# Optimization experiments

Measured on AMD Instinct MI355X. Metric: run time of the kernel, lower is better.

The kernel has to match this reference:

```python
import jax, jax.numpy as jnp
import numpy as np

N_HEAD = 16
D_MODEL = 1024
D_HEAD = D_MODEL // N_HEAD
B, T = 2, 2048


def setup_inputs() -> dict:
    key = jax.random.key(0)
    k1, k2, k3 = jax.random.split(key, 3)
    x = jax.random.normal(k1, (B, T, D_MODEL), dtype=jnp.float32)
    w_attn = jax.random.normal(k2, (3 * D_MODEL, D_MODEL), dtype=jnp.float32) * (D_MODEL ** -0.5)
    w_proj = jax.random.normal(k3, (D_MODEL, D_MODEL), dtype=jnp.float32) * (D_MODEL ** -0.5)
    return {"x": x, "w_attn": w_attn, "w_proj": w_proj}


def _rms_norm(x):
    eps = jnp.asarray(jnp.finfo(x.dtype).eps, x.dtype)
    var = jnp.mean(jnp.square(x), axis=-1, keepdims=True)
    return x * jax.lax.rsqrt(var + eps)


def _rotate_half(x):
    x1, x2 = jnp.split(x, 2, axis=-1)
    return jnp.concatenate((-x2, x1), axis=-1)


def reference(x, w_attn, w_proj):
    Bx, Tx, C = x.shape
    qkv = jnp.einsum('btc,fc->btf', x, w_attn)  # [B,T,3C]
    q, k, v = jnp.split(qkv, 3, axis=-1)
    # [B, H, T, Dh]
    q = q.reshape(Bx, Tx, N_HEAD, D_HEAD).transpose(0, 2, 1, 3)
    k = k.reshape(Bx, Tx, N_HEAD, D_HEAD).transpose(0, 2, 1, 3)
    v = v.reshape(Bx, Tx, N_HEAD, D_HEAD).transpose(0, 2, 1, 3)
    # QK RMSNorm (no learned weight)
    q = _rms_norm(q)
    k = _rms_norm(k)
    # Rotary embedding over full d_head: freqs tiled twice
    inv_freq = 1.0 / (10000.0 ** (jnp.arange(0, D_HEAD, 2, dtype=jnp.float32) / D_HEAD))
    t = jnp.arange(Tx, dtype=jnp.float32)
    freqs = jnp.einsum('i,j->ij', t, inv_freq)  # [T, Dh/2]
    emb = jnp.concatenate((freqs, freqs), axis=-1)  # [T, Dh]
    cos = jnp.cos(emb)[None, None, :, :]
    sin = jnp.sin(emb)[None, None, :, :]
    q = q * cos + _rotate_half(q) * sin
    k = k * cos + _rotate_half(k) * sin
    # Causal SDPA
    scale = D_HEAD ** -0.5
    scores = jnp.einsum('bhqd,bhkd->bhqk', q, k) * scale
    causal = jnp.tril(jnp.ones((Tx, Tx), dtype=bool))
    scores = jnp.where(causal[None, None], scores, jnp.asarray(-jnp.inf, scores.dtype))
    attn = jax.nn.softmax(scores, axis=-1)
    y = jnp.einsum('bhqk,bhkd->bhqd', attn, v)
    y = y.transpose(0, 2, 1, 3).reshape(Bx, Tx, C)
    return jnp.einsum('btc,oc->bto', y, w_proj)
```

## Files before the change

### kernel.cpp

```cpp
#include <hip/hip_runtime.h>
#include <cstdint>
#include <cstddef>


typedef short bf16x8 __attribute__((ext_vector_type(8)));
typedef short bf16x4 __attribute__((ext_vector_type(4)));
typedef float floatx4 __attribute__((ext_vector_type(4)));
typedef float floatx2 __attribute__((ext_vector_type(2)));
typedef unsigned short ushortx8 __attribute__((ext_vector_type(8)));
typedef unsigned short ushortx4 __attribute__((ext_vector_type(4)));
typedef unsigned int uintx2 __attribute__((ext_vector_type(2)));

#define DEVI __device__ __forceinline__

DEVI float bf2f(unsigned short u) {
    unsigned int x = ((unsigned int)u) << 16;
    return __builtin_bit_cast(float, x);
}
DEVI unsigned short f2bf(float f) {
    unsigned int u = __builtin_bit_cast(unsigned int, f);
    u += 0x7fffu + ((u >> 16) & 1u);
    return (unsigned short)(u >> 16);
}
DEVI unsigned int pkbf2(float a, float b) {
    unsigned int ua = __builtin_bit_cast(unsigned int, a) + 0x8000u;
    unsigned int ub = __builtin_bit_cast(unsigned int, b) + 0x8000u;
    return __builtin_amdgcn_perm(ub, ua, 0x07060302);
}

DEVI void glds16(const unsigned short* g, unsigned short* l) {
    __builtin_amdgcn_global_load_lds(
        (const __attribute__((address_space(1))) unsigned int*)g,
        (__attribute__((address_space(3))) unsigned int*)l, 16, 0, 0);
}

DEVI void cast8(unsigned short* dst, const float* src) {
    floatx4 a = *(const floatx4*)src;
    floatx4 b = *(const floatx4*)(src + 4);
    ushortx8 o;
    o[0] = f2bf(a[0]); o[1] = f2bf(a[1]); o[2] = f2bf(a[2]); o[3] = f2bf(a[3]);
    o[4] = f2bf(b[0]); o[5] = f2bf(b[1]); o[6] = f2bf(b[2]); o[7] = f2bf(b[3]);
    *(ushortx8*)dst = o;
}

__global__ __launch_bounds__(256)
void cast_inputs(const float* __restrict__ x, const float* __restrict__ wa,
                 const float* __restrict__ wp,
                 unsigned short* __restrict__ xb, unsigned short* __restrict__ wab,
                 unsigned short* __restrict__ wpb, float* __restrict__ ropetab)
{
    size_t g = (size_t)blockIdx.x * 256 + threadIdx.x;
    size_t stride = (size_t)gridDim.x * 256;
    for (size_t i = g; i < (4194304 / 8); i += stride) cast8(xb  + i * 8, x  + i * 8);
    for (size_t i = g; i < (3145728 / 8); i += stride) cast8(wab + i * 8, wa + i * 8);
    for (size_t i = g; i < (1048576 / 8); i += stride) cast8(wpb + i * 8, wp + i * 8);
    for (size_t i = g; i < 65536; i += stride) {
        int t = (int)(i >> 5), f = (int)(i & 31);
        float ang = (float)t * __expf(-(float)f * 0.28782313662425572f);
        float sn, cs;
        __sincosf(ang, &sn, &cs);
        ropetab[2 * i]     = cs;
        ropetab[2 * i + 1] = sn;
    }
}

__global__ __launch_bounds__(512, 2)
void gemm_qkv_8ph(const unsigned short* __restrict__ A,
                  const unsigned short* __restrict__ B,
                  const float* __restrict__ ropetab,
                  unsigned short* __restrict__ Cqk,
                  unsigned short* __restrict__ Vt)
{
    __shared__ __align__(16) unsigned short lds[2][2][256 * 64];

    const int tid  = threadIdx.x;
    const int lane = tid & 63;
    const int w    = tid >> 6;
    const int wm   = w >> 2;
    const int wn   = w & 3;
    const int quad = lane >> 4;
    const int lm   = lane & 15;

    const int lin = blockIdx.y * 12 + blockIdx.x;
    const int s   = (lin & 7) * 24 + (lin >> 3);
    const int m0  = (s / 12) * 256;
    const int n0  = (s % 12) * 256;

    const int srow = tid >> 3;
    const int scol = (((tid & 7) ^ ((tid >> 3) & 7)) * 8);
    const int ldst = w * 512;

#define STG_A(u, WBi, kq) glds16(&A[(size_t)(m0 + (u) * 64 + srow) * 1024 + (kq) + scol], \
                                 &lds[WBi][0][(u) * 4096 + ldst])
#define STG_B(u, WBi, kq) glds16(&B[(size_t)(n0 + (u) * 64 + srow) * 1024 + (kq) + scol], \
                                 &lds[WBi][1][(u) * 4096 + ldst])
#define RD_A(RBi, rrow, kk) (*(const bf16x8*)&lds[RBi][0][(rrow) * 64 + ((((kk) * 4 + quad) ^ ((rrow) & 7)) * 8)])
#define RD_B(RBi, rrow, kk) (*(const bf16x8*)&lds[RBi][1][(rrow) * 64 + ((((kk) * 4 + quad) ^ ((rrow) & 7)) * 8)])

    floatx4 acc[8][4] = {};
    bf16x8 afr[4][2];
    bf16x8 bfr[4][2];

#define MQ(MB, JB)                                                              \
  do {                                                                          \
    _Pragma("unroll")                                                           \
    for (int kk = 0; kk < 2; ++kk)                                              \
      _Pragma("unroll")                                                         \
      for (int mi = 0; mi < 4; ++mi)                                            \
        _Pragma("unroll")                                                       \
        for (int j2 = 0; j2 < 2; ++j2)                                          \
          acc[(MB) + mi][(JB) + j2] = __builtin_amdgcn_mfma_f32_16x16x32_bf16(  \
              afr[mi][kk], bfr[(JB) + j2][kk], acc[(MB) + mi][(JB) + j2], 0, 0, 0); \
  } while (0)

#define TILE(RBi, WBi, KT, LASTF)                                               \
  do {                                                                          \
    const int kn = ((KT) + 1) * 64;                                             \
    if (!(LASTF)) { STG_B(0, WBi, kn); STG_B(1, WBi, kn); }                     \
    _Pragma("unroll")                                                           \
    for (int kk = 0; kk < 2; ++kk) {                                            \
      _Pragma("unroll")                                                         \
      for (int mi = 0; mi < 4; ++mi)                                            \
        afr[mi][kk] = RD_A(RBi, wm * 128 + mi * 16 + lm, kk);                   \
      _Pragma("unroll")                                                         \
      for (int j2 = 0; j2 < 2; ++j2)                                            \
        bfr[j2][kk] = RD_B(RBi, wn * 64 + j2 * 16 + lm, kk);                    \
    }                                                                           \
    asm volatile("s_waitcnt lgkmcnt(8)" ::: "memory");                          \
    __builtin_amdgcn_s_barrier();                                               \
    asm volatile("s_waitcnt lgkmcnt(0)" ::: "memory");                          \
    __builtin_amdgcn_s_setprio(1); MQ(0, 0); __builtin_amdgcn_s_setprio(0);     \
    __builtin_amdgcn_s_barrier();                                               \
    if (!(LASTF)) { STG_B(2, WBi, kn); STG_B(3, WBi, kn); }                     \
    _Pragma("unroll")                                                           \
    for (int kk = 0; kk < 2; ++kk)                                              \
      _Pragma("unroll")                                                         \
      for (int j2 = 0; j2 < 2; ++j2)                                            \
        bfr[2 + j2][kk] = RD_B(RBi, wn * 64 + (2 + j2) * 16 + lm, kk);          \
    if (!(LASTF)) { asm volatile("s_waitcnt vmcnt(4)" ::: "memory"); }          \
    else          { asm volatile("s_waitcnt vmcnt(0)" ::: "memory"); }          \
    __builtin_amdgcn_s_barrier();                                               \
    asm volatile("s_waitcnt lgkmcnt(0)" ::: "memory");                          \
    __builtin_amdgcn_s_setprio(1); MQ(0, 2); __builtin_amdgcn_s_setprio(0);     \
    __builtin_amdgcn_s_barrier();                                               \
    if (!(LASTF)) { STG_A(0, WBi, kn); STG_A(2, WBi, kn); }                     \
    _Pragma("unroll")                                                           \
    for (int kk = 0; kk < 2; ++kk)                                              \
      _Pragma("unroll")                                                         \
      for (int mi = 0; mi < 4; ++mi)                                            \
        afr[mi][kk] = RD_A(RBi, wm * 128 + 64 + mi * 16 + lm, kk);              \
    __builtin_amdgcn_s_barrier();                                               \
    asm volatile("s_waitcnt lgkmcnt(0)" ::: "memory");                          \
    __builtin_amdgcn_s_setprio(1); MQ(4, 2); __builtin_amdgcn_s_setprio(0);     \
    __builtin_amdgcn_s_barrier();                                               \
    if (!(LASTF)) { STG_A(1, WBi, kn); STG_A(3, WBi, kn);                       \
                    asm volatile("s_waitcnt vmcnt(2)" ::: "memory"); }          \
    __builtin_amdgcn_s_barrier();                                               \
    __builtin_amdgcn_s_setprio(1); MQ(4, 0); __builtin_amdgcn_s_setprio(0);     \
    __builtin_amdgcn_s_barrier();                                               \
  } while (0)

    STG_B(0, 0, 0); STG_B(1, 0, 0); STG_B(2, 0, 0); STG_B(3, 0, 0);
    STG_A(0, 0, 0); STG_A(2, 0, 0); STG_A(1, 0, 0); STG_A(3, 0, 0);
    asm volatile("s_waitcnt vmcnt(2)" ::: "memory");
    __builtin_amdgcn_s_barrier();

    for (int kt = 0; kt < 14; kt += 2) {
        TILE(0, 1, kt, false);
        TILE(1, 0, kt + 1, false);
    }
    TILE(0, 1, 14, false);
    TILE(1, 0, 15, true);

    const bool is_v = (n0 + wn * 64) >= 2048;
    if (!is_v) {
        const floatx2* rtab = (const floatx2*)ropetab;
        #pragma unroll
        for (int mi = 0; mi < 8; ++mi) {
            float rn[4];
            #pragma unroll
            for (int r = 0; r < 4; ++r) {
                float ss = 0.0f;
                #pragma unroll
                for (int j = 0; j < 4; ++j) ss += acc[mi][j][r] * acc[mi][j][r];
                ss += __shfl_xor(ss, 1, 64);
                ss += __shfl_xor(ss, 2, 64);
                ss += __shfl_xor(ss, 4, 64);
                ss += __shfl_xor(ss, 8, 64);
                rn[r] = rsqrtf(ss * (1.0f / 64.0f) + 1.1920929e-07f);
            }
            #pragma unroll
            for (int r = 0; r < 4; ++r) {
                int row = m0 + wm * 128 + mi * 16 + quad * 4 + r;
                int t = row & 2047;
                floatx2 cs0 = rtab[t * 32 + lm];
                floatx2 cs1 = rtab[t * 32 + 16 + lm];
                float g = rn[r];
                #pragma unroll
                for (int j = 0; j < 4; ++j) {
                    int d = j * 16 + lm;
                    float cs = (j & 1) ? cs1[0] : cs0[0];
                    float sn = (j & 1) ? cs1[1] : cs0[1];
                    float v  = acc[mi][j][r] * g;
                    float vp = acc[mi][j ^ 2][r] * g;
                    float sgn = (d < 32) ? -1.0f : 1.0f;
                    Cqk[(size_t)row * 2048 + (n0 + wn * 64 + d)] =
                        f2bf(v * cs + sgn * vp * sn);
                }
            }
        }
    } else {
        #pragma unroll
        for (int mi = 0; mi < 8; ++mi)
            #pragma unroll
            for (int j = 0; j < 4; ++j) {
                int col  = n0 + wn * 64 + j * 16 + lm;
                int row0 = m0 + wm * 128 + mi * 16 + quad * 4;
                int bq = row0 >> 11, t0 = row0 & 2047;
                ushortx4 pk;
                #pragma unroll
                for (int r = 0; r < 4; ++r) pk[r] = f2bf(acc[mi][j][r]);
                *(ushortx4*)&Vt[((size_t)(bq * 1024 + (col - 2048))) * 2048 + t0] = pk;
            }
    }
#undef TILE
#undef MQ
#undef RD_A
#undef RD_B
#undef STG_A
#undef STG_B
}

template <int BN, int BK>
__global__ __launch_bounds__(256)
void gemm_bt(const unsigned short* __restrict__ A, const unsigned short* __restrict__ B,
             float* __restrict__ Cf, int M, int N, int K)
{
    constexpr int WCOLS = (BN == 128) ? 2 : 1;
    constexpr int WROWS = 4 / WCOLS;
    constexpr int MI    = 128 / (16 * WROWS);
    constexpr int LPR   = BK / 8;
    constexpr int RPI   = 64 / LPR;

    __shared__ __align__(16) unsigned short As[128 * BK];
    __shared__ __align__(16) unsigned short Bs[BN * BK];

    const int tid  = threadIdx.x;
    const int lane = tid & 63;
    const int w    = tid >> 6;
    const int wm   = w / WCOLS, wn = w % WCOLS;
    const int quad = lane >> 4;
    const int lm   = lane & 15;
    const int m0 = blockIdx.y * 128;
    const int n0 = blockIdx.x * BN;
    const int sr = lane / LPR;
    const int sc = (lane % LPR) * 8;

    floatx4 acc[MI][4] = {};

    for (int k0 = 0; k0 < K; k0 += BK) {
        __syncthreads();
        #pragma unroll
        for (int i = 0; i < 32 / RPI; ++i) {
            int r = w * 32 + i * RPI;
            glds16(&A[(size_t)(m0 + r + sr) * K + k0 + sc], &As[r * BK]);
        }
        #pragma unroll
        for (int i = 0; i < (BN / 4) / RPI; ++i) {
            int r = w * (BN / 4) + i * RPI;
            glds16(&B[(size_t)(n0 + r + sr) * K + k0 + sc], &Bs[r * BK]);
        }
        __syncthreads();

        #pragma unroll
        for (int kk = 0; kk < BK / 32; ++kk) {
            bf16x8 a[MI];
            #pragma unroll
            for (int i = 0; i < MI; ++i)
                a[i] = *(const bf16x8*)&As[(wm * (16 * MI) + i * 16 + lm) * BK + kk * 32 + quad * 8];
            #pragma unroll
            for (int j = 0; j < 4; ++j) {
                bf16x8 b = *(const bf16x8*)&Bs[(wn * 64 + j * 16 + lm) * BK + kk * 32 + quad * 8];
                #pragma unroll
                for (int i = 0; i < MI; ++i)
                    acc[i][j] = __builtin_amdgcn_mfma_f32_16x16x32_bf16(a[i], b, acc[i][j], 0, 0, 0);
            }
        }
    }

    #pragma unroll
    for (int i = 0; i < MI; ++i)
        #pragma unroll
        for (int j = 0; j < 4; ++j) {
            int col  = n0 + wn * 64 + j * 16 + lm;
            int row0 = m0 + wm * (16 * MI) + i * 16 + quad * 4;
            #pragma unroll
            for (int r = 0; r < 4; ++r)
                Cf[(size_t)(row0 + r) * N + col] = acc[i][j][r];
        }
}

#define ATTN_STEP(KSc, VSc, KSn, VSn, KT, DG, LAST)                            \
  do {                                                                         \
    if (!(LAST)) {                                                             \
      *(ushortx8*)&(KSn)[r0 * LD + pc] = kreg0;                                \
      *(ushortx8*)&(KSn)[r1 * LD + pc] = kreg1;                                \
      *(ushortx8*)&(VSn)[r0 * LD + pc] = vreg0;                                \
      *(ushortx8*)&(VSn)[r1 * LD + pc] = vreg1;                                \
      if ((KT) + 2 <= qt) {                                                    \
        kreg0 = *(const ushortx8*)kp0; kreg1 = *(const ushortx8*)kp1;          \
        vreg0 = *(const ushortx8*)vp0; vreg1 = *(const ushortx8*)vp1;          \
        kp0 += (size_t)64 * 2048; kp1 += (size_t)64 * 2048;                    \
        vp0 += 64; vp1 += 64;                                                  \
      }                                                                        \
    }                                                                          \
    \
    bf16x4 vb0[4], vb1[4], vb2[4], vb3[4];                                     \
    _Pragma("unroll")                                                          \
    for (int jd = 0; jd < 4; ++jd) {                                           \
      vb0[jd] = *(const bf16x4*)&(VSc)[(jd * 16 + lm) * LD +  0 + quad * 4];   \
      vb1[jd] = *(const bf16x4*)&(VSc)[(jd * 16 + lm) * LD + 16 + quad * 4];   \
      vb2[jd] = *(const bf16x4*)&(VSc)[(jd * 16 + lm) * LD + 32 + quad * 4];   \
      vb3[jd] = *(const bf16x4*)&(VSc)[(jd * 16 + lm) * LD + 48 + quad * 4];   \
    }                                                                          \
    floatx4 sa[4] = {};                                                        \
    _Pragma("unroll")                                                          \
    for (int kk = 0; kk < 2; ++kk)                                             \
      _Pragma("unroll")                                                        \
      for (int j = 0; j < 4; ++j) {                                            \
        bf16x8 kf = *(const bf16x8*)&(KSc)[(j * 16 + lm) * LD + kk * 32 + quad * 8]; \
        sa[j] = __builtin_amdgcn_mfma_f32_16x16x32_bf16(kf, qf[kk], sa[j], 0, 0, 0); \
      }                                                                        \
    bf16x4 pa[4];                                                              \
    _Pragma("unroll")                                                          \
    for (int j = 0; j < 4; ++j) {                                              \
      float p0 = exp2f(sa[j][0] * c1 - c2);                                    \
      float p1 = exp2f(sa[j][1] * c1 - c2);                                    \
      float p2 = exp2f(sa[j][2] * c1 - c2);                                    \
      float p3 = exp2f(sa[j][3] * c1 - c2);                                    \
      if (DG) {                                                                \
        int kb = (KT) * 64 + j * 16 + quad * 4;                                \
        if (kb + 0 > qrow) p0 = 0.0f;                                          \
        if (kb + 1 > qrow) p1 = 0.0f;                                          \
        if (kb + 2 > qrow) p2 = 0.0f;                                          \
        if (kb + 3 > qrow) p3 = 0.0f;                                          \
      }                                                                        \
      uintx2 pk;                                                               \
      pk[0] = pkbf2(p0, p1);                                                   \
      pk[1] = pkbf2(p2, p3);                                                   \
      pa[j] = __builtin_bit_cast(bf16x4, pk);                                  \
    }                                                                          \
    _Pragma("unroll")                                                          \
    for (int j = 0; j < 4; ++j)                                                \
      l_acc = __builtin_amdgcn_mfma_f32_16x16x16bf16_1k(pa[j], ones4, l_acc, 0, 0, 0); \
    _Pragma("unroll")                                                          \
    for (int jd = 0; jd < 4; ++jd) {                                           \
      o[jd] = __builtin_amdgcn_mfma_f32_16x16x16bf16_1k(pa[0], vb0[jd], o[jd], 0, 0, 0); \
      o[jd] = __builtin_amdgcn_mfma_f32_16x16x16bf16_1k(pa[1], vb1[jd], o[jd], 0, 0, 0); \
      o[jd] = __builtin_amdgcn_mfma_f32_16x16x16bf16_1k(pa[2], vb2[jd], o[jd], 0, 0, 0); \
      o[jd] = __builtin_amdgcn_mfma_f32_16x16x16bf16_1k(pa[3], vb3[jd], o[jd], 0, 0, 0); \
    }                                                                          \
    if (!(LAST)) __syncthreads();                                              \
  } while (0)

__global__ __launch_bounds__(256)
void attention(const unsigned short* __restrict__ qk,
               const unsigned short* __restrict__ Vt,
               unsigned short* __restrict__ Y)
{
    constexpr int LD = 72;
    __shared__ __align__(16) unsigned short QPs[64 * LD];
    __shared__ __align__(16) unsigned short Ks0[64 * LD];
    __shared__ __align__(16) unsigned short Ks1[64 * LD];
    __shared__ __align__(16) unsigned short Vs0[64 * LD];
    __shared__ __align__(16) unsigned short Vs1[64 * LD];

    const int tid  = threadIdx.x;
    const int lane = tid & 63;
    const int w    = tid >> 6;
    const int quad = lane >> 4;
    const int lm   = lane & 15;

    const int bh = blockIdx.x;
    const int qt = 31 - blockIdx.y;
    const int b  = bh >> 4, h = bh & 15;
    const int q0 = qt * 64;
    const int qrow = q0 + w * 16 + lm;

    const int r0 = tid >> 3, r1 = r0 + 32, pc = (tid & 7) * 8;
    const unsigned short* kp0 = qk + (size_t)b * 2048 * 2048 + 1024 + h * 64
                              + (size_t)r0 * 2048 + pc;
    const unsigned short* kp1 = kp0 + (size_t)32 * 2048;
    const unsigned short* vp0 = Vt + (size_t)bh * 64 * 2048 + (size_t)r0 * 2048 + pc;
    const unsigned short* vp1 = vp0 + (size_t)32 * 2048;

    #pragma unroll
    for (int i = 0; i < 2; ++i) {
        int c = i * 256 + tid, row = c >> 3, col = (c & 7) * 8;
        *(ushortx8*)&QPs[row * LD + col] =
            *(const ushortx8*)&qk[((size_t)(b * 2048 + q0 + row)) * 2048 + h * 64 + col];
    }

    ushortx8 kreg0 = *(const ushortx8*)kp0, kreg1 = *(const ushortx8*)kp1;
    ushortx8 vreg0 = *(const ushortx8*)vp0, vreg1 = *(const ushortx8*)vp1;
    kp0 += (size_t)64 * 2048; kp1 += (size_t)64 * 2048;
    vp0 += 64; vp1 += 64;
    *(ushortx8*)&Ks0[r0 * LD + pc] = kreg0;
    *(ushortx8*)&Ks0[r1 * LD + pc] = kreg1;
    *(ushortx8*)&Vs0[r0 * LD + pc] = vreg0;
    *(ushortx8*)&Vs0[r1 * LD + pc] = vreg1;
    if (qt >= 1) {
        kreg0 = *(const ushortx8*)kp0; kreg1 = *(const ushortx8*)kp1;
        vreg0 = *(const ushortx8*)vp0; vreg1 = *(const ushortx8*)vp1;
        kp0 += (size_t)64 * 2048; kp1 += (size_t)64 * 2048;
        vp0 += 64; vp1 += 64;
    }
    __syncthreads();

    bf16x8 qf[2];
    #pragma unroll
    for (int kk = 0; kk < 2; ++kk)
        qf[kk] = *(const bf16x8*)&QPs[(w * 16 + lm) * LD + kk * 32 + quad * 8];

    bf16x4 ones4;
    #pragma unroll
    for (int i = 0; i < 4; ++i) ones4[i] = (short)0x3F80;

    floatx4 o[4] = {};
    floatx4 l_acc = {};
    const float c1 = 0.125f * 1.44269504f;
    const float c2 = 8.0f   * 1.44269504f;

    int kt = 0;
    for (; kt + 1 < qt; kt += 2) {
        ATTN_STEP(Ks0, Vs0, Ks1, Vs1, kt,     false, false);
        ATTN_STEP(Ks1, Vs1, Ks0, Vs0, kt + 1, false, false);
    }
    if (kt < qt) {
        ATTN_STEP(Ks0, Vs0, Ks1, Vs1, kt, false, false);
        ATTN_STEP(Ks1, Vs1, Ks0, Vs0, qt, true, true);
    } else {
        ATTN_STEP(Ks0, Vs0, Ks1, Vs1, qt, true, true);
    }

    float rinv[4];
    #pragma unroll
    for (int r = 0; r < 4; ++r) rinv[r] = 1.0f / l_acc[r];

    #pragma unroll
    for (int jd = 0; jd < 4; ++jd) {
        int colg = h * 64 + jd * 16 + lm;
        #pragma unroll
        for (int r = 0; r < 4; ++r) {
            int rowg = q0 + w * 16 + quad * 4 + r;
            Y[((size_t)(b * 2048 + rowg)) * 1024 + colg] = f2bf(o[jd][r] * rinv[r]);
        }
    }
}

extern "C" void kernel_launch(void* const* d_in, const int* in_sizes, int n_in,
                              void* d_out, int out_size, void* d_ws, size_t ws_size,
                              hipStream_t stream)
{
    const float* x      = (const float*)d_in[0];
    const float* w_attn = (const float*)d_in[1];
    const float* w_proj = (const float*)d_in[2];
    float* out = (float*)d_out;

    unsigned short* qkbuf = (unsigned short*)d_ws;
    unsigned short* Vtb   = qkbuf + (size_t)4096 * 2048;
    unsigned short* y     = Vtb   + (size_t)32 * 64 * 2048;
    unsigned short* wpb   = y     + (size_t)4096 * 1024;
    unsigned short* xb  = (unsigned short*)d_out;
    unsigned short* wab = xb + (size_t)4096 * 1024;
    float* ropetab = (float*)(wab + (size_t)3072 * 1024);

    dim3 blk(256);
    cast_inputs<<<dim3(1024), blk, 0, stream>>>(x, w_attn, w_proj, xb, wab, wpb, ropetab);
    gemm_qkv_8ph<<<dim3(12, 16), dim3(512), 0, stream>>>(xb, wab, ropetab, qkbuf, Vtb);
    attention<<<dim3(32, 32), blk, 0, stream>>>(qkbuf, Vtb, y);
    gemm_bt<64, 64>
        <<<dim3(16, 32), blk, 0, stream>>>(y, wpb, out, 4096, 1024, 1024);
}
```

Measured before the change: 175.9 us.

## Split attention KV tiles across warps with direct-to-LDS loads and swizzled layout

```diff
diff --git a/kernel.cpp b/kernel.cpp
--- a/kernel.cpp
+++ b/kernel.cpp
@@ -13,10 +13,6 @@
 
 #define DEVI __device__ __forceinline__
 
-DEVI float bf2f(unsigned short u) {
-    unsigned int x = ((unsigned int)u) << 16;
-    return __builtin_bit_cast(float, x);
-}
 DEVI unsigned short f2bf(float f) {
     unsigned int u = __builtin_bit_cast(unsigned int, f);
     u += 0x7fffu + ((u >> 16) & 1u);
@@ -174,6 +170,7 @@
 
     const bool is_v = (n0 + wn * 64) >= 2048;
     if (!is_v) {
+        const float qsc = ((n0 + wn * 64) < 1024) ? 0.18033688011112043f : 1.0f;
         const floatx2* rtab = (const floatx2*)ropetab;
         #pragma unroll
         for (int mi = 0; mi < 8; ++mi) {
@@ -205,7 +202,7 @@
                     float vp = acc[mi][j ^ 2][r] * g;
                     float sgn = (d < 32) ? -1.0f : 1.0f;
                     Cqk[(size_t)row * 2048 + (n0 + wn * 64 + d)] =
-                        f2bf(v * cs + sgn * vp * sn);
+                        f2bf((v * cs + sgn * vp * sn) * qsc);
                 }
             }
         }
@@ -300,136 +297,153 @@
         }
 }
 
-#define ATTN_STEP(KSc, VSc, KSn, VSn, KT, DG, LAST)                            \
+#define GRP(OT, LT, QT, g, KT, DG)                                             \
+  {                                                                            \
+    floatx4 sa = {};                                                           \
+    sa = __builtin_amdgcn_mfma_f32_16x16x32_bf16(kf0, QT[0], sa, 0, 0, 0);     \
+    sa = __builtin_amdgcn_mfma_f32_16x16x32_bf16(kf1, QT[1], sa, 0, 0, 0);     \
+    float p0 = exp2f(sa[0]);                                                   \
+    float p1 = exp2f(sa[1]);                                                   \
+    float p2 = exp2f(sa[2]);                                                   \
+    float p3 = exp2f(sa[3]);                                                   \
+    if (DG) {                                                                  \
+      int kb = (KT) * 64 + w * 16 + quad * 4;                                  \
+      int qr = q0 + (g) * 16 + lm;                                             \
+      if (kb + 0 > qr) p0 = 0.0f;                                              \
+      if (kb + 1 > qr) p1 = 0.0f;                                              \
+      if (kb + 2 > qr) p2 = 0.0f;                                              \
+      if (kb + 3 > qr) p3 = 0.0f;                                              \
+    }                                                                          \
+    uintx2 pk;                                                                 \
+    pk[0] = pkbf2(p0, p1);                                                     \
+    pk[1] = pkbf2(p2, p3);                                                     \
+    bf16x4 pa = __builtin_bit_cast(bf16x4, pk);                                \
+    LT = __builtin_amdgcn_mfma_f32_16x16x16bf16_1k(pa, ones4, LT, 0, 0, 0);    \
+    OT[0] = __builtin_amdgcn_mfma_f32_16x16x16bf16_1k(pa, vb0, OT[0], 0, 0, 0);\
+    OT[1] = __builtin_amdgcn_mfma_f32_16x16x16bf16_1k(pa, vb1, OT[1], 0, 0, 0);\
+    OT[2] = __builtin_amdgcn_mfma_f32_16x16x16bf16_1k(pa, vb2, OT[2], 0, 0, 0);\
+    OT[3] = __builtin_amdgcn_mfma_f32_16x16x16bf16_1k(pa, vb3, OT[3], 0, 0, 0);\
+  }
+
+#define ATTN_STEP(KS, VS, KSn, VSn, KT, DG, LAST)                              \
   do {                                                                         \
     if (!(LAST)) {                                                             \
-      *(ushortx8*)&(KSn)[r0 * LD + pc] = kreg0;                                \
-      *(ushortx8*)&(KSn)[r1 * LD + pc] = kreg1;                                \
-      *(ushortx8*)&(VSn)[r0 * LD + pc] = vreg0;                                \
-      *(ushortx8*)&(VSn)[r1 * LD + pc] = vreg1;                                \
-      if ((KT) + 2 <= qt) {                                                    \
-        kreg0 = *(const ushortx8*)kp0; kreg1 = *(const ushortx8*)kp1;          \
-        vreg0 = *(const ushortx8*)vp0; vreg1 = *(const ushortx8*)vp1;          \
-        kp0 += (size_t)64 * 2048; kp1 += (size_t)64 * 2048;                    \
-        vp0 += 64; vp1 += 64;                                                  \
-      }                                                                        \
+      const size_t tn = (size_t)((KT) + 1);                                    \
+      glds16(kg + tn * 131072,         (KSn) + w * 512);                       \
+      glds16(kg + tn * 131072 + 65536, (KSn) + 2048 + w * 512);                \
+      glds16(vg + tn * 64,             (VSn) + w * 512);                       \
+      glds16(vg + tn * 64 + 65536,     (VSn) + 2048 + w * 512);                \
     }                                                                          \
-    \
-    bf16x4 vb0[4], vb1[4], vb2[4], vb3[4];                                     \
+    bf16x8 kf0 = *(const bf16x8*)&(KS)[kfo0];                                  \
+    bf16x8 kf1 = *(const bf16x8*)&(KS)[kfo1];                                  \
+    bf16x4 vb0 = *(const bf16x4*)&(VS)[vbo0];                                  \
+    bf16x4 vb1 = *(const bf16x4*)&(VS)[vbo1];                                  \
+    bf16x4 vb2 = *(const bf16x4*)&(VS)[vbo2];                                  \
+    bf16x4 vb3 = *(const bf16x4*)&(VS)[vbo3];                                  \
+    GRP(oA, lA, qfA, 0, KT, DG)                                                \
+    GRP(oB, lB, qfB, 1, KT, DG)                                                \
+    GRP(oC, lC, qfC, 2, KT, DG)                                                \
+    GRP(oD, lD, qfD, 3, KT, DG)                                                \
+    if (!(LAST)) __syncthreads();                                              \
+  } while (0)
+
+#define OWR1(S, OT, g)                                                         \
+  _Pragma("unroll")                                                            \
+  for (int jd = 0; jd < 4; ++jd)                                               \
     _Pragma("unroll")                                                          \
-    for (int jd = 0; jd < 4; ++jd) {                                           \
-      vb0[jd] = *(const bf16x4*)&(VSc)[(jd * 16 + lm) * LD +  0 + quad * 4];   \
-      vb1[jd] = *(const bf16x4*)&(VSc)[(jd * 16 + lm) * LD + 16 + quad * 4];   \
-      vb2[jd] = *(const bf16x4*)&(VSc)[(jd * 16 + lm) * LD + 32 + quad * 4];   \
-      vb3[jd] = *(const bf16x4*)&(VSc)[(jd * 16 + lm) * LD + 48 + quad * 4];   \
-    }                                                                          \
-    floatx4 sa[4] = {};                                                        \
+    for (int r = 0; r < 4; ++r)                                                \
+      (S)[((g) * 16 + quad * 4 + r) * 64 + jd * 16 + lm] = OT[jd][r];
+#define OWR(S) { OWR1(S, oA, 0) OWR1(S, oB, 1) OWR1(S, oC, 2) OWR1(S, oD, 3) }
+#define OAC1(S, OT, g)                                                         \
+  _Pragma("unroll")                                                            \
+  for (int jd = 0; jd < 4; ++jd)                                               \
     _Pragma("unroll")                                                          \
-    for (int kk = 0; kk < 2; ++kk)                                             \
-      _Pragma("unroll")                                                        \
-      for (int j = 0; j < 4; ++j) {                                            \
-        bf16x8 kf = *(const bf16x8*)&(KSc)[(j * 16 + lm) * LD + kk * 32 + quad * 8]; \
-        sa[j] = __builtin_amdgcn_mfma_f32_16x16x32_bf16(kf, qf[kk], sa[j], 0, 0, 0); \
-      }                                                                        \
-    bf16x4 pa[4];                                                              \
+    for (int r = 0; r < 4; ++r)                                                \
+      OT[jd][r] += (S)[((g) * 16 + quad * 4 + r) * 64 + jd * 16 + lm];
+#define OAC(S) { OAC1(S, oA, 0) OAC1(S, oB, 1) OAC1(S, oC, 2) OAC1(S, oD, 3) }
+
+#define YWR(OT, g)                                                             \
+  {                                                                            \
+    float rv[4];                                                               \
     _Pragma("unroll")                                                          \
-    for (int j = 0; j < 4; ++j) {                                              \
-      float p0 = exp2f(sa[j][0] * c1 - c2);                                    \
-      float p1 = exp2f(sa[j][1] * c1 - c2);                                    \
-      float p2 = exp2f(sa[j][2] * c1 - c2);                                    \
-      float p3 = exp2f(sa[j][3] * c1 - c2);                                    \
-      if (DG) {                                                                \
-        int kb = (KT) * 64 + j * 16 + quad * 4;                                \
-        if (kb + 0 > qrow) p0 = 0.0f;                                          \
-        if (kb + 1 > qrow) p1 = 0.0f;                                          \
-        if (kb + 2 > qrow) p2 = 0.0f;                                          \
-        if (kb + 3 > qrow) p3 = 0.0f;                                          \
-      }                                                                        \
-      uintx2 pk;                                                               \
-      pk[0] = pkbf2(p0, p1);                                                   \
-      pk[1] = pkbf2(p2, p3);                                                   \
-      pa[j] = __builtin_bit_cast(bf16x4, pk);                                  \
+    for (int r = 0; r < 4; ++r) {                                              \
+      int qi = (g) * 16 + quad * 4 + r;                                        \
+      rv[r] = 1.0f / (lsc[qi] + lsc[64 + qi] + lsc[128 + qi] + lsc[192 + qi]); \
     }                                                                          \
     _Pragma("unroll")                                                          \
-    for (int j = 0; j < 4; ++j)                                                \
-      l_acc = __builtin_amdgcn_mfma_f32_16x16x16bf16_1k(pa[j], ones4, l_acc, 0, 0, 0); \
-    _Pragma("unroll")                                                          \
-    for (int jd = 0; jd < 4; ++jd) {                                           \
-      o[jd] = __builtin_amdgcn_mfma_f32_16x16x16bf16_1k(pa[0], vb0[jd], o[jd], 0, 0, 0); \
-      o[jd] = __builtin_amdgcn_mfma_f32_16x16x16bf16_1k(pa[1], vb1[jd], o[jd], 0, 0, 0); \
-      o[jd] = __builtin_amdgcn_mfma_f32_16x16x16bf16_1k(pa[2], vb2[jd], o[jd], 0, 0, 0); \
-      o[jd] = __builtin_amdgcn_mfma_f32_16x16x16bf16_1k(pa[3], vb3[jd], o[jd], 0, 0, 0); \
-    }                                                                          \
-    if (!(LAST)) __syncthreads();                                              \
-  } while (0)
-
-__global__ __launch_bounds__(256)
+    for (int jd = 0; jd < 4; ++jd)                                             \
+      _Pragma("unroll")                                                        \
+      for (int r = 0; r < 4; ++r)                                              \
+        Y[((size_t)(b * 2048 + q0 + (g) * 16 + quad * 4 + r)) * 1024 +         \
+          h * 64 + jd * 16 + lm] = f2bf(OT[jd][r] * rv[r]);                    \
+  }
+
+__global__ __launch_bounds__(256, 2)
 void attention(const unsigned short* __restrict__ qk,
                const unsigned short* __restrict__ Vt,
                unsigned short* __restrict__ Y)
 {
-    constexpr int LD = 72;
-    __shared__ __align__(16) unsigned short QPs[64 * LD];
-    __shared__ __align__(16) unsigned short Ks0[64 * LD];
-    __shared__ __align__(16) unsigned short Ks1[64 * LD];
-    __shared__ __align__(16) unsigned short Vs0[64 * LD];
-    __shared__ __align__(16) unsigned short Vs1[64 * LD];
+    __shared__ __align__(16) unsigned short smem[20480];
+    unsigned short* const QPs = smem;
+    unsigned short* const Ks0 = smem + 4096;
+    unsigned short* const Ks1 = smem + 8192;
+    unsigned short* const Vs0 = smem + 12288;
+    unsigned short* const Vs1 = smem + 16384;
+    float* const lsc  = (float*)smem;
+    float* const ScrA = (float*)(smem + 4096);
+    float* const ScrB = (float*)(smem + 12288);
 
     const int tid  = threadIdx.x;
     const int lane = tid & 63;
     const int w    = tid >> 6;
     const int quad = lane >> 4;
     const int lm   = lane & 15;
+    const int sx   = lm & 7;
 
     const int bh = blockIdx.x;
     const int qt = 31 - blockIdx.y;
     const int b  = bh >> 4, h = bh & 15;
     const int q0 = qt * 64;
-    const int qrow = q0 + w * 16 + lm;
-
-    const int r0 = tid >> 3, r1 = r0 + 32, pc = (tid & 7) * 8;
-    const unsigned short* kp0 = qk + (size_t)b * 2048 * 2048 + 1024 + h * 64
-                              + (size_t)r0 * 2048 + pc;
-    const unsigned short* kp1 = kp0 + (size_t)32 * 2048;
-    const unsigned short* vp0 = Vt + (size_t)bh * 64 * 2048 + (size_t)r0 * 2048 + pc;
-    const unsigned short* vp1 = vp0 + (size_t)32 * 2048;
-
+
+    const int kfo0 = (w * 16 + lm) * 64 + ((quad)     ^ sx) * 8;
+    const int kfo1 = (w * 16 + lm) * 64 + ((4 + quad) ^ sx) * 8;
+    const int vch  = (w * 2 + (quad >> 1)) ^ sx;
+    const int vbo0 = (0 * 16 + lm) * 64 + vch * 8 + (quad & 1) * 4;
+    const int vbo1 = (1 * 16 + lm) * 64 + vch * 8 + (quad & 1) * 4;
+    const int vbo2 = (2 * 16 + lm) * 64 + vch * 8 + (quad & 1) * 4;
+    const int vbo3 = (3 * 16 + lm) * 64 + vch * 8 + (quad & 1) * 4;
+
+    const int srow = tid >> 3;
+    const int scol = ((tid & 7) ^ (srow & 7)) * 8;
+    const unsigned short* kg = qk + (size_t)b * 4194304 + 1024 + h * 64
+                             + (size_t)srow * 2048 + scol;
+    const unsigned short* vg = Vt + (size_t)bh * 131072 + (size_t)srow * 2048 + scol;
+    const unsigned short* qg = qk + ((size_t)(b * 2048 + q0 + srow)) * 2048
+                             + h * 64 + scol;
+
+    glds16(qg,         QPs + w * 512);
+    glds16(qg + 65536, QPs + 2048 + w * 512);
+    glds16(kg,         Ks0 + w * 512);
+    glds16(kg + 65536, Ks0 + 2048 + w * 512);
+    glds16(vg,         Vs0 + w * 512);
+    glds16(vg + 65536, Vs0 + 2048 + w * 512);
+    __syncthreads();
+
+    bf16x8 qfA[2], qfB[2], qfC[2], qfD[2];
     #pragma unroll
-    for (int i = 0; i < 2; ++i) {
-        int c = i * 256 + tid, row = c >> 3, col = (c & 7) * 8;
-        *(ushortx8*)&QPs[row * LD + col] =
-            *(const ushortx8*)&qk[((size_t)(b * 2048 + q0 + row)) * 2048 + h * 64 + col];
-    }
-
-    ushortx8 kreg0 = *(const ushortx8*)kp0, kreg1 = *(const ushortx8*)kp1;
-    ushortx8 vreg0 = *(const ushortx8*)vp0, vreg1 = *(const ushortx8*)vp1;
-    kp0 += (size_t)64 * 2048; kp1 += (size_t)64 * 2048;
-    vp0 += 64; vp1 += 64;
-    *(ushortx8*)&Ks0[r0 * LD + pc] = kreg0;
-    *(ushortx8*)&Ks0[r1 * LD + pc] = kreg1;
-    *(ushortx8*)&Vs0[r0 * LD + pc] = vreg0;
-    *(ushortx8*)&Vs0[r1 * LD + pc] = vreg1;
-    if (qt >= 1) {
-        kreg0 = *(const ushortx8*)kp0; kreg1 = *(const ushortx8*)kp1;
-        vreg0 = *(const ushortx8*)vp0; vreg1 = *(const ushortx8*)vp1;
-        kp0 += (size_t)64 * 2048; kp1 += (size_t)64 * 2048;
-        vp0 += 64; vp1 += 64;
-    }
-    __syncthreads();
-
-    bf16x8 qf[2];
-    #pragma unroll
-    for (int kk = 0; kk < 2; ++kk)
-        qf[kk] = *(const bf16x8*)&QPs[(w * 16 + lm) * LD + kk * 32 + quad * 8];
+    for (int kk = 0; kk < 2; ++kk) {
+        qfA[kk] = *(const bf16x8*)&QPs[(0 * 16 + lm) * 64 + ((kk * 4 + quad) ^ sx) * 8];
+        qfB[kk] = *(const bf16x8*)&QPs[(1 * 16 + lm) * 64 + ((kk * 4 + quad) ^ sx) * 8];
+        qfC[kk] = *(const bf16x8*)&QPs[(2 * 16 + lm) * 64 + ((kk * 4 + quad) ^ sx) * 8];
+        qfD[kk] = *(const bf16x8*)&QPs[(3 * 16 + lm) * 64 + ((kk * 4 + quad) ^ sx) * 8];
+    }
 
     bf16x4 ones4;
     #pragma unroll
     for (int i = 0; i < 4; ++i) ones4[i] = (short)0x3F80;
 
-    floatx4 o[4] = {};
-    floatx4 l_acc = {};
-    const float c1 = 0.125f * 1.44269504f;
-    const float c2 = 8.0f   * 1.44269504f;
+    floatx4 oA[4] = {}, oB[4] = {}, oC[4] = {}, oD[4] = {};
+    floatx4 lA = {}, lB = {}, lC = {}, lD = {};
 
     int kt = 0;
     for (; kt + 1 < qt; kt += 2) {
@@ -443,18 +457,30 @@
         ATTN_STEP(Ks0, Vs0, Ks1, Vs1, qt, true, true);
     }
 
-    float rinv[4];
-    #pragma unroll
-    for (int r = 0; r < 4; ++r) rinv[r] = 1.0f / l_acc[r];
-
-    #pragma unroll
-    for (int jd = 0; jd < 4; ++jd) {
-        int colg = h * 64 + jd * 16 + lm;
+    __syncthreads();
+    if (lm == 0) {
         #pragma unroll
         for (int r = 0; r < 4; ++r) {
-            int rowg = q0 + w * 16 + quad * 4 + r;
-            Y[((size_t)(b * 2048 + rowg)) * 1024 + colg] = f2bf(o[jd][r] * rinv[r]);
+            lsc[w * 64 +  0 + quad * 4 + r] = lA[r];
+            lsc[w * 64 + 16 + quad * 4 + r] = lB[r];
+            lsc[w * 64 + 32 + quad * 4 + r] = lC[r];
+            lsc[w * 64 + 48 + quad * 4 + r] = lD[r];
         }
+    }
+    if (w == 1) { OWR(ScrA) }
+    if (w == 3) { OWR(ScrB) }
+    __syncthreads();
+    if (w == 0) { OAC(ScrA) }
+    if (w == 2) { OAC(ScrB) }
+    __syncthreads();
+    if (w == 2) { OWR(ScrA) }
+    __syncthreads();
+    if (w == 0) {
+        OAC(ScrA)
+        YWR(oA, 0)
+        YWR(oB, 1)
+        YWR(oC, 2)
+        YWR(oD, 3)
     }
 }
 
```

New measurement: 177.7 us. No clear change (+1.0%).
